# Performance work log

Measured on AMD Instinct MI355X. Metric: run time of the kernel, lower is better.

Reference implementation:

```python
import jax, jax.numpy as jnp
import numpy as np

B, S, D = 2, 2048, 1024
H = 16
HD = D // H


def setup_inputs() -> dict:
    key = jax.random.key(0)
    k1, k2, k3 = jax.random.split(key, 3)
    x = jax.random.normal(k1, (B, S, D), dtype=jnp.float32)
    mask = jnp.ones((B, S), dtype=jnp.float32)
    # Conv1D = Linear; torch init: weight std=0.002, bias zeros. Store as [in, out].
    W_qkv = 0.002 * jax.random.normal(k2, (D, 3 * D), dtype=jnp.float32)
    b_qkv = jnp.zeros((3 * D,), dtype=jnp.float32)
    W_o = 0.002 * jax.random.normal(k3, (D, D), dtype=jnp.float32)
    b_o = jnp.zeros((D,), dtype=jnp.float32)
    return {"x": x, "mask": mask, "W_qkv": W_qkv, "b_qkv": b_qkv, "W_o": W_o, "b_o": b_o}


def reference(x, mask, W_qkv, b_qkv, W_o, b_o):
    b, s, d = x.shape
    qkv = (x @ W_qkv + b_qkv).reshape(b, s, 3, H, HD)
    q, k, v = qkv[:, :, 0], qkv[:, :, 1], qkv[:, :, 2]  # [b,s,h,hd]
    w = jnp.einsum('bshd,bzhd->bhsz', q, k)
    w = w / jnp.sqrt(jnp.float32(HD))  # scale=True
    # padding mask applied on both query and key axes via log-add
    logm = jnp.log(mask)
    w = w + logm[:, None, :, None] + logm[:, None, None, :]
    # causal (bidir=False): log(tril) = 0 on/below diag, -inf above
    causal = jnp.tril(jnp.ones((s, s), dtype=jnp.float32))
    w = w + jnp.log(causal)[None, None]
    w = jax.nn.softmax(w, axis=-1)
    vw = jnp.einsum('bhsz,bzhd->bshd', w, v).reshape(b, s, d)
    return vw @ W_o + b_o
```

## Files before the change

kernel.cpp:

```cpp
#include <hip/hip_runtime.h>
#include <math.h>

#define BB 2
#define SS 2048
#define DD 1024
#define HH 16
#define HDIM 64
#define NQKV 3072

typedef __attribute__((ext_vector_type(8))) short bf16x8;
typedef __attribute__((ext_vector_type(4))) float f32x4;
typedef __attribute__((ext_vector_type(4))) unsigned short us4;

__device__ __forceinline__ unsigned short f2bf(float f) {
    unsigned u = __float_as_uint(f);
    unsigned r = ((u >> 16) & 1u) + 0x7FFFu;
    return (unsigned short)((u + r) >> 16);
}

__device__ __forceinline__ int swz(int row, int col) {
    int b = row * 128 + col * 2;
    return b ^ ((row & 7) << 4);
}

#define GLOAD16(g, l)                                                  \
    __builtin_amdgcn_global_load_lds(                                  \
        (const __attribute__((address_space(1))) unsigned int*)(g),    \
        (__attribute__((address_space(3))) unsigned int*)(l), 16, 0, 0)

__global__ __launch_bounds__(256) void conv_x(const float* __restrict__ X,
                                              unsigned short* __restrict__ Xb) {
    const int i = blockIdx.x * 256 + threadIdx.x;
    float4 v = ((const float4*)X)[i];
    us4 w;
    w.x = f2bf(v.x); w.y = f2bf(v.y); w.z = f2bf(v.z); w.w = f2bf(v.w);
    ((us4*)Xb)[i] = w;
}

__global__ __launch_bounds__(256) void conv_wT(const float* __restrict__ W,
                                               unsigned short* __restrict__ WT,
                                               int N) {
    __shared__ unsigned short L[64][80];
    const int k0 = blockIdx.y * 64, n0 = blockIdx.x * 64;
    const int t = threadIdx.x;
    const int kr = t >> 4;
    const int nc = (t & 15) * 4;
#pragma unroll
    for (int p = 0; p < 4; ++p) {
        float4 v = *(const float4*)&W[(size_t)(k0 + kr + p * 16) * N + n0 + nc];
        L[nc + 0][kr + p * 16] = f2bf(v.x);
        L[nc + 1][kr + p * 16] = f2bf(v.y);
        L[nc + 2][kr + p * 16] = f2bf(v.z);
        L[nc + 3][kr + p * 16] = f2bf(v.w);
    }
    __syncthreads();
    const int r = t >> 2, c = (t & 3) * 16;
    *(bf16x8*)&WT[(size_t)(n0 + r) * DD + k0 + c] = *(bf16x8*)&L[r][c];
    *(bf16x8*)&WT[(size_t)(n0 + r) * DD + k0 + c + 8] = *(bf16x8*)&L[r][c + 8];
}

__global__ __launch_bounds__(256) void qkv_gemm(
        const unsigned short* __restrict__ A, const unsigned short* __restrict__ BT,
        const float* __restrict__ bias,
        unsigned short* __restrict__ Qp, unsigned short* __restrict__ Kp,
        unsigned short* __restrict__ Vt) {
    __shared__ unsigned short As[128 * 64];
    __shared__ unsigned short Bs[128 * 64];
    char* Ab = (char*)As;
    char* Bb = (char*)Bs;

    const int tid = threadIdx.x;
    const int lane = tid & 63, wave = tid >> 6;
    const int ln = lane & 15, hi = lane >> 4;
    const int wr = wave >> 1, wc = wave & 1;
    const int m0 = blockIdx.y * 128, n0 = blockIdx.x * 128;

    f32x4 acc[4][4];
#pragma unroll
    for (int i = 0; i < 4; ++i)
#pragma unroll
        for (int j = 0; j < 4; ++j) acc[i][j] = (f32x4){0.f, 0.f, 0.f, 0.f};

    for (int k0 = 0; k0 < DD; k0 += 64) {
        __syncthreads();
#pragma unroll
        for (int i = 0; i < 4; ++i) {
            const int d = tid * 16 + i * 4096;
            const int row = d >> 7;
            const int colb = (d & 127) ^ ((row & 7) << 4);
            GLOAD16(&A[(size_t)(m0 + row) * DD + k0 + (colb >> 1)], Ab + d);
            GLOAD16(&BT[(size_t)(n0 + row) * DD + k0 + (colb >> 1)], Bb + d);
        }
        __syncthreads();
#pragma unroll
        for (int kk = 0; kk < 2; ++kk) {
            bf16x8 af[4], bf[4];
#pragma unroll
            for (int mi = 0; mi < 4; ++mi)
                af[mi] = *(const bf16x8*)(Ab + swz(wr * 64 + mi * 16 + ln, kk * 32 + hi * 8));
#pragma unroll
            for (int ni = 0; ni < 4; ++ni)
                bf[ni] = *(const bf16x8*)(Bb + swz(wc * 64 + ni * 16 + ln, kk * 32 + hi * 8));
#pragma unroll
            for (int mi = 0; mi < 4; ++mi)
#pragma unroll
                for (int ni = 0; ni < 4; ++ni)
                    acc[mi][ni] = __builtin_amdgcn_mfma_f32_16x16x32_bf16(
                        af[mi], bf[ni], acc[mi][ni], 0, 0, 0);
        }
    }

    const int c = n0 >> 10;
#pragma unroll
    for (int ni = 0; ni < 4; ++ni) {
        const int n_g = n0 + wc * 64 + ni * 16 + ln;
        const float bv = bias[n_g];
        const int rem = n_g & 1023;
        const int h = rem >> 6;
        const int hd = rem & 63;
#pragma unroll
        for (int mi = 0; mi < 4; ++mi) {
            const int mbase = m0 + wr * 64 + mi * 16 + hi * 4;
            const int b = mbase >> 11;
            const int s = mbase & 2047;
            if (c == 2) {
                us4 w;
                w.x = f2bf(acc[mi][ni][0] + bv);
                w.y = f2bf(acc[mi][ni][1] + bv);
                w.z = f2bf(acc[mi][ni][2] + bv);
                w.w = f2bf(acc[mi][ni][3] + bv);
                *(us4*)&Vt[(((size_t)b * HH + h) * HDIM + hd) * SS + s] = w;
            } else {
                unsigned short* dst = (c == 0) ? Qp : Kp;
#pragma unroll
                for (int reg = 0; reg < 4; ++reg)
                    dst[(((size_t)b * HH + h) * SS + s + reg) * HDIM + hd] =
                        f2bf(acc[mi][ni][reg] + bv);
            }
        }
    }
}

__global__ __launch_bounds__(512) void flash_attn_mfma(
        const unsigned short* __restrict__ Qp, const unsigned short* __restrict__ Kp,
        const unsigned short* __restrict__ Vt, const float* __restrict__ mask,
        unsigned short* __restrict__ Ao) {
    __shared__ unsigned short Ks[2][64 * 64];
    __shared__ unsigned short VT[2][64 * 64];
    __shared__ unsigned short Pl[8][16 * 64];

    const int tid = threadIdx.x;
    const int lane = tid & 63, wave = tid >> 6;
    const int ln = lane & 15, hi = lane >> 4;
    const int qt = (int)gridDim.x - 1 - (int)blockIdx.x;
    const int h = blockIdx.y;
    const int bq = blockIdx.z;
    char* pb = (char*)Pl[wave];

    const size_t headoff = ((size_t)bq * HH + h) * SS * HDIM;
    const unsigned short* Kbase = Kp + headoff;
    const unsigned short* Vtbase = Vt + headoff;
    const float* mbase = mask + (size_t)bq * SS;

    const int qq = qt * 128 + wave * 16 + ln;
    const unsigned short* qsrc = Qp + headoff + (size_t)qq * HDIM;
    bf16x8 qa[2];
#pragma unroll
    for (int kk = 0; kk < 2; ++kk)
        qa[kk] = *(const bf16x8*)(qsrc + kk * 32 + hi * 8);

    f32x4 oacc[4];
#pragma unroll
    for (int i = 0; i < 4; ++i) oacc[i] = (f32x4){0.f, 0.f, 0.f, 0.f};
    float mrun = -3e38f, lrun = 0.f;
    const int qwmin = qt * 128 + wave * 16;

    const int srow = tid >> 3;
    const int d_lin = tid * 16;
    const int scolb = (d_lin & 127) ^ ((srow & 7) << 4);
    const int scol = scolb >> 1;

    const int tmax = 2 * qt + 1;
    GLOAD16(Kbase + (size_t)srow * HDIM + scol, (char*)Ks[0] + d_lin);
    GLOAD16(Vtbase + (size_t)srow * SS + scol, (char*)VT[0] + d_lin);

    int buf = 0;
    for (int t = 0; t <= tmax; ++t) {
        const int z0 = t * 64;
        __syncthreads();
        if (t < tmax) {
            const int zn = z0 + 64;
            GLOAD16(Kbase + (size_t)(zn + srow) * HDIM + scol, (char*)Ks[buf ^ 1] + d_lin);
            GLOAD16(Vtbase + (size_t)srow * SS + zn + scol, (char*)VT[buf ^ 1] + d_lin);
        }
        char* Kb = (char*)Ks[buf];
        char* Vb = (char*)VT[buf];

        f32x4 sacc[4];
#pragma unroll
        for (int i = 0; i < 4; ++i) sacc[i] = (f32x4){0.f, 0.f, 0.f, 0.f};
        __builtin_amdgcn_s_setprio(1);
#pragma unroll
        for (int kk = 0; kk < 2; ++kk)
#pragma unroll
            for (int ns = 0; ns < 4; ++ns) {
                bf16x8 kb = *(const bf16x8*)(Kb + swz(ns * 16 + ln, kk * 32 + hi * 8));
                sacc[ns] = __builtin_amdgcn_mfma_f32_16x16x32_bf16(kb, qa[kk], sacc[ns], 0, 0, 0);
            }
        __builtin_amdgcn_s_setprio(0);

        float4 mv4[4];
#pragma unroll
        for (int ns = 0; ns < 4; ++ns)
            mv4[ns] = *(const float4*)&mbase[z0 + ns * 16 + hi * 4];
        if (z0 + 63 > qwmin) {
            const int kvb = z0 + hi * 4;
#pragma unroll
            for (int ns = 0; ns < 4; ++ns)
#pragma unroll
                for (int reg = 0; reg < 4; ++reg)
                    if (kvb + ns * 16 + reg > qq) mv4[ns][reg] = 0.f;
        }

        float pm = -3e38f;
#pragma unroll
        for (int ns = 0; ns < 4; ++ns)
#pragma unroll
            for (int reg = 0; reg < 4; ++reg) pm = fmaxf(pm, sacc[ns][reg]);
        pm = fmaxf(pm, __shfl_xor(pm, 16));
        pm = fmaxf(pm, __shfl_xor(pm, 32));

        if (!__all(pm <= mrun + 64.f)) {
            const float mn = fmaxf(mrun, pm);
            const float al = __expf((mrun - mn) * 0.125f);
            float alr[4];
#pragma unroll
            for (int reg = 0; reg < 4; ++reg) alr[reg] = __shfl(al, hi * 4 + reg);
#pragma unroll
            for (int ns = 0; ns < 4; ++ns)
#pragma unroll
                for (int reg = 0; reg < 4; ++reg) oacc[ns][reg] *= alr[reg];
            lrun *= al;
            mrun = mn;
        }

        float sum = 0.f;
#pragma unroll
        for (int ns = 0; ns < 4; ++ns) {
#pragma unroll
            for (int reg = 0; reg < 4; ++reg) {
                float p = __expf((sacc[ns][reg] - mrun) * 0.125f) * mv4[ns][reg];
                sacc[ns][reg] = p;
                sum += p;
            }
        }
        sum += __shfl_xor(sum, 16);
        sum += __shfl_xor(sum, 32);
        lrun += sum;

#pragma unroll
        for (int ns = 0; ns < 4; ++ns) {
            us4 w;
            w.x = f2bf(sacc[ns][0]);
            w.y = f2bf(sacc[ns][1]);
            w.z = f2bf(sacc[ns][2]);
            w.w = f2bf(sacc[ns][3]);
            *(us4*)(pb + swz(ln, ns * 16 + hi * 4)) = w;
        }

        bf16x8 pa[2];
#pragma unroll
        for (int kk = 0; kk < 2; ++kk)
            pa[kk] = *(const bf16x8*)(pb + swz(ln, kk * 32 + hi * 8));
        __builtin_amdgcn_s_setprio(1);
#pragma unroll
        for (int ns = 0; ns < 4; ++ns)
#pragma unroll
            for (int kk = 0; kk < 2; ++kk) {
                bf16x8 vb = *(const bf16x8*)(Vb + swz(ns * 16 + ln, kk * 32 + hi * 8));
                oacc[ns] = __builtin_amdgcn_mfma_f32_16x16x32_bf16(pa[kk], vb, oacc[ns], 0, 0, 0);
            }
        __builtin_amdgcn_s_setprio(0);
        buf ^= 1;
    }

    const float inv = 1.f / lrun;
    float invr[4];
#pragma unroll
    for (int reg = 0; reg < 4; ++reg) invr[reg] = __shfl(inv, hi * 4 + reg);
#pragma unroll
    for (int ns = 0; ns < 4; ++ns) {
        const int hd = ns * 16 + ln;
#pragma unroll
        for (int reg = 0; reg < 4; ++reg) {
            const int s = qt * 128 + wave * 16 + hi * 4 + reg;
            Ao[((size_t)bq * SS + s) * DD + h * HDIM + hd] = f2bf(oacc[ns][reg] * invr[reg]);
        }
    }
}

__global__ __launch_bounds__(256) void out_gemm(
        const unsigned short* __restrict__ A, const unsigned short* __restrict__ BT,
        const float* __restrict__ bias, float* __restrict__ Out) {
    __shared__ unsigned short As[128 * 64];
    __shared__ unsigned short Bs[128 * 64];
    char* Ab = (char*)As;
    char* Bb = (char*)Bs;

    const int tid = threadIdx.x;
    const int lane = tid & 63, wave = tid >> 6;
    const int ln = lane & 15, hi = lane >> 4;
    const int wr = wave >> 1, wc = wave & 1;
    const int m0 = blockIdx.y * 128, n0 = blockIdx.x * 128;

    f32x4 acc[4][4];
#pragma unroll
    for (int i = 0; i < 4; ++i)
#pragma unroll
        for (int j = 0; j < 4; ++j) acc[i][j] = (f32x4){0.f, 0.f, 0.f, 0.f};

    for (int k0 = 0; k0 < DD; k0 += 64) {
        __syncthreads();
#pragma unroll
        for (int i = 0; i < 4; ++i) {
            const int d = tid * 16 + i * 4096;
            const int row = d >> 7;
            const int colb = (d & 127) ^ ((row & 7) << 4);
            GLOAD16(&A[(size_t)(m0 + row) * DD + k0 + (colb >> 1)], Ab + d);
            GLOAD16(&BT[(size_t)(n0 + row) * DD + k0 + (colb >> 1)], Bb + d);
        }
        __syncthreads();
#pragma unroll
        for (int kk = 0; kk < 2; ++kk) {
            bf16x8 af[4], bf[4];
#pragma unroll
            for (int mi = 0; mi < 4; ++mi)
                af[mi] = *(const bf16x8*)(Ab + swz(wr * 64 + mi * 16 + ln, kk * 32 + hi * 8));
#pragma unroll
            for (int ni = 0; ni < 4; ++ni)
                bf[ni] = *(const bf16x8*)(Bb + swz(wc * 64 + ni * 16 + ln, kk * 32 + hi * 8));
#pragma unroll
            for (int mi = 0; mi < 4; ++mi)
#pragma unroll
                for (int ni = 0; ni < 4; ++ni)
                    acc[mi][ni] = __builtin_amdgcn_mfma_f32_16x16x32_bf16(
                        af[mi], bf[ni], acc[mi][ni], 0, 0, 0);
        }
    }

#pragma unroll
    for (int ni = 0; ni < 4; ++ni) {
        const int n_g = n0 + wc * 64 + ni * 16 + ln;
        const float bv = bias[n_g];
#pragma unroll
        for (int mi = 0; mi < 4; ++mi) {
            const int mbase = m0 + wr * 64 + mi * 16 + hi * 4;
#pragma unroll
            for (int reg = 0; reg < 4; ++reg)
                Out[(size_t)(mbase + reg) * DD + n_g] = acc[mi][ni][reg] + bv;
        }
    }
}

extern "C" void kernel_launch(void* const* d_in, const int* in_sizes, int n_in,
                              void* d_out, int out_size, void* d_ws, size_t ws_size,
                              hipStream_t stream) {
    const float* x     = (const float*)d_in[0];
    const float* mask  = (const float*)d_in[1];
    const float* W_qkv = (const float*)d_in[2];
    const float* b_qkv = (const float*)d_in[3];
    const float* W_o   = (const float*)d_in[4];
    const float* b_o   = (const float*)d_in[5];
    float* out = (float*)d_out;

    unsigned short* ws = (unsigned short*)d_ws;
    const size_t per = (size_t)BB * HH * SS * HDIM;
    unsigned short* Qp  = ws;
    unsigned short* Kp  = Qp + per;
    unsigned short* Vt  = Kp + per;
    unsigned short* Aob = Vt + per;
    unsigned short* Xb  = Aob + per;
    unsigned short* WqT = Xb + (size_t)BB * SS * DD;
    unsigned short* WoT = WqT + (size_t)NQKV * DD;

    conv_x<<<dim3((BB * SS * DD) / 1024), 256, 0, stream>>>(x, Xb);
    conv_wT<<<dim3(NQKV / 64, DD / 64), 256, 0, stream>>>(W_qkv, WqT, NQKV);
    conv_wT<<<dim3(DD / 64, DD / 64), 256, 0, stream>>>(W_o, WoT, DD);

    qkv_gemm<<<dim3(NQKV / 128, (BB * SS) / 128), 256, 0, stream>>>(
        Xb, WqT, b_qkv, Qp, Kp, Vt);
    flash_attn_mfma<<<dim3(SS / 128, HH, BB), 512, 0, stream>>>(
        Qp, Kp, Vt, mask, Aob);
    out_gemm<<<dim3(DD / 128, (BB * SS) / 128), 256, 0, stream>>>(
        Aob, WoT, b_o, out);
}
```

Baseline: 229.9 us.

## Pair causal query tiles per block and merge conversion kernels into one launch

```diff
diff --git a/kernel.cpp b/kernel.cpp
--- a/kernel.cpp
+++ b/kernel.cpp
@@ -28,21 +28,34 @@
         (const __attribute__((address_space(1))) unsigned int*)(g),    \
         (__attribute__((address_space(3))) unsigned int*)(l), 16, 0, 0)
 
-__global__ __launch_bounds__(256) void conv_x(const float* __restrict__ X,
-                                              unsigned short* __restrict__ Xb) {
-    const int i = blockIdx.x * 256 + threadIdx.x;
-    float4 v = ((const float4*)X)[i];
-    us4 w;
-    w.x = f2bf(v.x); w.y = f2bf(v.y); w.z = f2bf(v.z); w.w = f2bf(v.w);
-    ((us4*)Xb)[i] = w;
-}
-
-__global__ __launch_bounds__(256) void conv_wT(const float* __restrict__ W,
-                                               unsigned short* __restrict__ WT,
-                                               int N) {
+__global__ __launch_bounds__(256) void conv_all(
+        const float* __restrict__ X, const float* __restrict__ Wq,
+        const float* __restrict__ Wo,
+        unsigned short* __restrict__ Xb, unsigned short* __restrict__ WqT,
+        unsigned short* __restrict__ WoT) {
     __shared__ unsigned short L[64][80];
-    const int k0 = blockIdx.y * 64, n0 = blockIdx.x * 64;
+    const int bid = blockIdx.x;
     const int t = threadIdx.x;
+    if (bid < 4096) {
+        const int i = bid * 256 + t;
+        float4 v = ((const float4*)X)[i];
+        us4 w;
+        w.x = f2bf(v.x); w.y = f2bf(v.y); w.z = f2bf(v.z); w.w = f2bf(v.w);
+        ((us4*)Xb)[i] = w;
+        return;
+    }
+    const float* W;
+    unsigned short* WT;
+    int N, n0, k0;
+    if (bid < 4864) {
+        const int idx = bid - 4096;
+        W = Wq; WT = WqT; N = NQKV;
+        n0 = (idx % 48) * 64; k0 = (idx / 48) * 64;
+    } else {
+        const int idx = bid - 4864;
+        W = Wo; WT = WoT; N = DD;
+        n0 = (idx % 16) * 64; k0 = (idx / 16) * 64;
+    }
     const int kr = t >> 4;
     const int nc = (t & 15) * 4;
 #pragma unroll
@@ -141,18 +154,18 @@
     }
 }
 
-__global__ __launch_bounds__(512) void flash_attn_mfma(
+__global__ __launch_bounds__(256) void flash_attn_mfma(
         const unsigned short* __restrict__ Qp, const unsigned short* __restrict__ Kp,
         const unsigned short* __restrict__ Vt, const float* __restrict__ mask,
         unsigned short* __restrict__ Ao) {
     __shared__ unsigned short Ks[2][64 * 64];
-    __shared__ unsigned short VT[2][64 * 64];
-    __shared__ unsigned short Pl[8][16 * 64];
+    __shared__ unsigned short VTs[2][64 * 64];
+    __shared__ unsigned short Pl[4][16 * 64];
 
     const int tid = threadIdx.x;
     const int lane = tid & 63, wave = tid >> 6;
     const int ln = lane & 15, hi = lane >> 4;
-    const int qt = (int)gridDim.x - 1 - (int)blockIdx.x;
+    const int pr = blockIdx.x;
     const int h = blockIdx.y;
     const int bq = blockIdx.z;
     char* pb = (char*)Pl[wave];
@@ -162,139 +175,150 @@
     const unsigned short* Vtbase = Vt + headoff;
     const float* mbase = mask + (size_t)bq * SS;
 
-    const int qq = qt * 128 + wave * 16 + ln;
-    const unsigned short* qsrc = Qp + headoff + (size_t)qq * HDIM;
-    bf16x8 qa[2];
-#pragma unroll
-    for (int kk = 0; kk < 2; ++kk)
-        qa[kk] = *(const bf16x8*)(qsrc + kk * 32 + hi * 8);
-
-    f32x4 oacc[4];
-#pragma unroll
-    for (int i = 0; i < 4; ++i) oacc[i] = (f32x4){0.f, 0.f, 0.f, 0.f};
-    float mrun = -3e38f, lrun = 0.f;
-    const int qwmin = qt * 128 + wave * 16;
-
-    const int srow = tid >> 3;
-    const int d_lin = tid * 16;
-    const int scolb = (d_lin & 127) ^ ((srow & 7) << 4);
-    const int scol = scolb >> 1;
-
-    const int tmax = 2 * qt + 1;
-    GLOAD16(Kbase + (size_t)srow * HDIM + scol, (char*)Ks[0] + d_lin);
-    GLOAD16(Vtbase + (size_t)srow * SS + scol, (char*)VT[0] + d_lin);
-
-    int buf = 0;
-    for (int t = 0; t <= tmax; ++t) {
-        const int z0 = t * 64;
+    for (int mem = 0; mem < 2; ++mem) {
+        const int qt = mem ? (31 - pr) : pr;
+        const int qbase = qt * 64;
+        const int qq = qbase + wave * 16 + ln;
+
+        const unsigned short* qsrc = Qp + headoff + (size_t)qq * HDIM;
+        bf16x8 qa[2];
+#pragma unroll
+        for (int kk = 0; kk < 2; ++kk)
+            qa[kk] = *(const bf16x8*)(qsrc + kk * 32 + hi * 8);
+
+        f32x4 oacc[4];
+#pragma unroll
+        for (int i = 0; i < 4; ++i) oacc[i] = (f32x4){0.f, 0.f, 0.f, 0.f};
+        float mrun = -3e38f, lrun = 0.f;
+
         __syncthreads();
-        if (t < tmax) {
-            const int zn = z0 + 64;
-            GLOAD16(Kbase + (size_t)(zn + srow) * HDIM + scol, (char*)Ks[buf ^ 1] + d_lin);
-            GLOAD16(Vtbase + (size_t)srow * SS + zn + scol, (char*)VT[buf ^ 1] + d_lin);
-        }
-        char* Kb = (char*)Ks[buf];
-        char* Vb = (char*)VT[buf];
-
-        f32x4 sacc[4];
-#pragma unroll
-        for (int i = 0; i < 4; ++i) sacc[i] = (f32x4){0.f, 0.f, 0.f, 0.f};
-        __builtin_amdgcn_s_setprio(1);
-#pragma unroll
-        for (int kk = 0; kk < 2; ++kk)
+#pragma unroll
+        for (int c = 0; c < 2; ++c) {
+            const int d = tid * 16 + c * 4096;
+            const int row = d >> 7;
+            const int col = ((d & 127) ^ ((row & 7) << 4)) >> 1;
+            GLOAD16(Kbase + (size_t)row * HDIM + col, (char*)Ks[0] + d);
+            GLOAD16(Vtbase + (size_t)row * SS + col, (char*)VTs[0] + d);
+        }
+
+        int buf = 0;
+        for (int t = 0; t <= qt; ++t) {
+            const int z0 = t * 64;
+            __syncthreads();
+            if (t < qt) {
+                const int zn = z0 + 64;
+#pragma unroll
+                for (int c = 0; c < 2; ++c) {
+                    const int d = tid * 16 + c * 4096;
+                    const int row = d >> 7;
+                    const int col = ((d & 127) ^ ((row & 7) << 4)) >> 1;
+                    GLOAD16(Kbase + (size_t)(zn + row) * HDIM + col, (char*)Ks[buf ^ 1] + d);
+                    GLOAD16(Vtbase + (size_t)row * SS + zn + col, (char*)VTs[buf ^ 1] + d);
+                }
+            }
+            char* Kb = (char*)Ks[buf];
+            char* Vb = (char*)VTs[buf];
+
+            f32x4 sacc[4];
+#pragma unroll
+            for (int i = 0; i < 4; ++i) sacc[i] = (f32x4){0.f, 0.f, 0.f, 0.f};
+            __builtin_amdgcn_s_setprio(1);
+#pragma unroll
+            for (int kk = 0; kk < 2; ++kk)
+#pragma unroll
+                for (int ns = 0; ns < 4; ++ns) {
+                    bf16x8 kb = *(const bf16x8*)(Kb + swz(ns * 16 + ln, kk * 32 + hi * 8));
+                    sacc[ns] = __builtin_amdgcn_mfma_f32_16x16x32_bf16(kb, qa[kk], sacc[ns], 0, 0, 0);
+                }
+            __builtin_amdgcn_s_setprio(0);
+
+            float4 mv4[4];
+#pragma unroll
+            for (int ns = 0; ns < 4; ++ns)
+                mv4[ns] = *(const float4*)&mbase[z0 + ns * 16 + hi * 4];
+            if (t == qt) {
+                const int kvb = z0 + hi * 4;
+#pragma unroll
+                for (int ns = 0; ns < 4; ++ns)
+#pragma unroll
+                    for (int reg = 0; reg < 4; ++reg)
+                        if (kvb + ns * 16 + reg > qq) mv4[ns][reg] = 0.f;
+            }
+
+            float pm = -3e38f;
+#pragma unroll
+            for (int ns = 0; ns < 4; ++ns)
+#pragma unroll
+                for (int reg = 0; reg < 4; ++reg) pm = fmaxf(pm, sacc[ns][reg]);
+            pm = fmaxf(pm, __shfl_xor(pm, 16));
+            pm = fmaxf(pm, __shfl_xor(pm, 32));
+
+            if (!__all(pm <= mrun + 64.f)) {
+                const float mn = fmaxf(mrun, pm);
+                const float al = __expf((mrun - mn) * 0.125f);
+                float alr[4];
+#pragma unroll
+                for (int reg = 0; reg < 4; ++reg) alr[reg] = __shfl(al, hi * 4 + reg);
+#pragma unroll
+                for (int ns = 0; ns < 4; ++ns)
+#pragma unroll
+                    for (int reg = 0; reg < 4; ++reg) oacc[ns][reg] *= alr[reg];
+                lrun *= al;
+                mrun = mn;
+            }
+
+            float sum = 0.f;
 #pragma unroll
             for (int ns = 0; ns < 4; ++ns) {
-                bf16x8 kb = *(const bf16x8*)(Kb + swz(ns * 16 + ln, kk * 32 + hi * 8));
-                sacc[ns] = __builtin_amdgcn_mfma_f32_16x16x32_bf16(kb, qa[kk], sacc[ns], 0, 0, 0);
-            }
-        __builtin_amdgcn_s_setprio(0);
-
-        float4 mv4[4];
-#pragma unroll
-        for (int ns = 0; ns < 4; ++ns)
-            mv4[ns] = *(const float4*)&mbase[z0 + ns * 16 + hi * 4];
-        if (z0 + 63 > qwmin) {
-            const int kvb = z0 + hi * 4;
+#pragma unroll
+                for (int reg = 0; reg < 4; ++reg) {
+                    float p = __expf((sacc[ns][reg] - mrun) * 0.125f) * mv4[ns][reg];
+                    sacc[ns][reg] = p;
+                    sum += p;
+                }
+            }
+            sum += __shfl_xor(sum, 16);
+            sum += __shfl_xor(sum, 32);
+            lrun += sum;
+
+#pragma unroll
+            for (int ns = 0; ns < 4; ++ns) {
+                us4 w;
+                w.x = f2bf(sacc[ns][0]);
+                w.y = f2bf(sacc[ns][1]);
+                w.z = f2bf(sacc[ns][2]);
+                w.w = f2bf(sacc[ns][3]);
+                *(us4*)(pb + swz(ln, ns * 16 + hi * 4)) = w;
+            }
+
+            bf16x8 pa[2];
+#pragma unroll
+            for (int kk = 0; kk < 2; ++kk)
+                pa[kk] = *(const bf16x8*)(pb + swz(ln, kk * 32 + hi * 8));
+            __builtin_amdgcn_s_setprio(1);
 #pragma unroll
             for (int ns = 0; ns < 4; ++ns)
 #pragma unroll
-                for (int reg = 0; reg < 4; ++reg)
-                    if (kvb + ns * 16 + reg > qq) mv4[ns][reg] = 0.f;
-        }
-
-        float pm = -3e38f;
-#pragma unroll
-        for (int ns = 0; ns < 4; ++ns)
-#pragma unroll
-            for (int reg = 0; reg < 4; ++reg) pm = fmaxf(pm, sacc[ns][reg]);
-        pm = fmaxf(pm, __shfl_xor(pm, 16));
-        pm = fmaxf(pm, __shfl_xor(pm, 32));
-
-        if (!__all(pm <= mrun + 64.f)) {
-            const float mn = fmaxf(mrun, pm);
-            const float al = __expf((mrun - mn) * 0.125f);
-            float alr[4];
-#pragma unroll
-            for (int reg = 0; reg < 4; ++reg) alr[reg] = __shfl(al, hi * 4 + reg);
-#pragma unroll
-            for (int ns = 0; ns < 4; ++ns)
-#pragma unroll
-                for (int reg = 0; reg < 4; ++reg) oacc[ns][reg] *= alr[reg];
-            lrun *= al;
-            mrun = mn;
-        }
-
-        float sum = 0.f;
+                for (int kk = 0; kk < 2; ++kk) {
+                    bf16x8 vb = *(const bf16x8*)(Vb + swz(ns * 16 + ln, kk * 32 + hi * 8));
+                    oacc[ns] = __builtin_amdgcn_mfma_f32_16x16x32_bf16(pa[kk], vb, oacc[ns], 0, 0, 0);
+                }
+            __builtin_amdgcn_s_setprio(0);
+            buf ^= 1;
+        }
+
+        const float inv = 1.f / lrun;
+        float invr[4];
+#pragma unroll
+        for (int reg = 0; reg < 4; ++reg) invr[reg] = __shfl(inv, hi * 4 + reg);
 #pragma unroll
         for (int ns = 0; ns < 4; ++ns) {
+            const int hd = ns * 16 + ln;
 #pragma unroll
             for (int reg = 0; reg < 4; ++reg) {
-                float p = __expf((sacc[ns][reg] - mrun) * 0.125f) * mv4[ns][reg];
-                sacc[ns][reg] = p;
-                sum += p;
-            }
-        }
-        sum += __shfl_xor(sum, 16);
-        sum += __shfl_xor(sum, 32);
-        lrun += sum;
-
-#pragma unroll
-        for (int ns = 0; ns < 4; ++ns) {
-            us4 w;
-            w.x = f2bf(sacc[ns][0]);
-            w.y = f2bf(sacc[ns][1]);
-            w.z = f2bf(sacc[ns][2]);
-            w.w = f2bf(sacc[ns][3]);
-            *(us4*)(pb + swz(ln, ns * 16 + hi * 4)) = w;
-        }
-
-        bf16x8 pa[2];
-#pragma unroll
-        for (int kk = 0; kk < 2; ++kk)
-            pa[kk] = *(const bf16x8*)(pb + swz(ln, kk * 32 + hi * 8));
-        __builtin_amdgcn_s_setprio(1);
-#pragma unroll
-        for (int ns = 0; ns < 4; ++ns)
-#pragma unroll
-            for (int kk = 0; kk < 2; ++kk) {
-                bf16x8 vb = *(const bf16x8*)(Vb + swz(ns * 16 + ln, kk * 32 + hi * 8));
-                oacc[ns] = __builtin_amdgcn_mfma_f32_16x16x32_bf16(pa[kk], vb, oacc[ns], 0, 0, 0);
-            }
-        __builtin_amdgcn_s_setprio(0);
-        buf ^= 1;
-    }
-
-    const float inv = 1.f / lrun;
-    float invr[4];
-#pragma unroll
-    for (int reg = 0; reg < 4; ++reg) invr[reg] = __shfl(inv, hi * 4 + reg);
-#pragma unroll
-    for (int ns = 0; ns < 4; ++ns) {
-        const int hd = ns * 16 + ln;
-#pragma unroll
-        for (int reg = 0; reg < 4; ++reg) {
-            const int s = qt * 128 + wave * 16 + hi * 4 + reg;
-            Ao[((size_t)bq * SS + s) * DD + h * HDIM + hd] = f2bf(oacc[ns][reg] * invr[reg]);
+                const int s = qbase + wave * 16 + hi * 4 + reg;
+                Ao[((size_t)bq * SS + s) * DD + h * HDIM + hd] = f2bf(oacc[ns][reg] * invr[reg]);
+            }
         }
     }
 }
@@ -383,13 +407,11 @@
     unsigned short* WqT = Xb + (size_t)BB * SS * DD;
     unsigned short* WoT = WqT + (size_t)NQKV * DD;
 
-    conv_x<<<dim3((BB * SS * DD) / 1024), 256, 0, stream>>>(x, Xb);
-    conv_wT<<<dim3(NQKV / 64, DD / 64), 256, 0, stream>>>(W_qkv, WqT, NQKV);
-    conv_wT<<<dim3(DD / 64, DD / 64), 256, 0, stream>>>(W_o, WoT, DD);
-
+    conv_all<<<dim3(4096 + 768 + 256), 256, 0, stream>>>(
+        x, W_qkv, W_o, Xb, WqT, WoT);
     qkv_gemm<<<dim3(NQKV / 128, (BB * SS) / 128), 256, 0, stream>>>(
         Xb, WqT, b_qkv, Qp, Kp, Vt);
-    flash_attn_mfma<<<dim3(SS / 128, HH, BB), 512, 0, stream>>>(
+    flash_attn_mfma<<<dim3(16, HH, BB), 256, 0, stream>>>(
         Qp, Kp, Vt, mask, Aob);
     out_gemm<<<dim3(DD / 128, (BB * SS) / 128), 256, 0, stream>>>(
         Aob, WoT, b_o, out);
```

Result: faster. 211.6 us (-7.9%).
